# Kernel tuning notes

Measured on AMD Instinct MI355X. Metric: run time of the kernel, lower is better.

Reference implementation:

```python
import jax, jax.numpy as jnp
import numpy as np
import math

SEQ_LEN = 2048
D_MODEL = 1024
N_HEAD = 16
BATCH = 4


def setup_inputs() -> dict:
    key = jax.random.key(0)
    ks = jax.random.split(key, 12)
    D, T = D_MODEL, SEQ_LEN
    lin_bound = 1.0 / math.sqrt(D)  # torch nn.Linear default init
    xav_bound = math.sqrt(6.0 / (T + T))  # xavier_uniform for wbias
    u = lambda k, shape, b: jax.random.uniform(k, shape, jnp.float32, -b, b)
    return {
        "x": jax.random.normal(ks[0], (BATCH, T, D), jnp.float32),
        "dummy": 0,
        "Wq": u(ks[1], (D, D), lin_bound), "bq": u(ks[2], (D,), lin_bound),
        "Wk": u(ks[3], (D, D), lin_bound), "bk": u(ks[4], (D,), lin_bound),
        "Wv": u(ks[5], (D, D), lin_bound), "bv": u(ks[6], (D,), lin_bound),
        "Wo": u(ks[7], (D, D), lin_bound), "bo": u(ks[8], (D,), lin_bound),
        "wbias": u(ks[9], (T, T), xav_bound),
    }


def reference(x, dummy, Wq, bq, Wk, bk, Wv, bv, Wo, bo, wbias):
    B, T, D = x.shape
    H = N_HEAD
    dh = D // H

    def proj(W, b):
        # nn.Linear: x @ W.T + b, then view(B,T,H,dh) -> (B,H,T,dh)
        y = jnp.einsum('btd,ed->bte', x, W) + b
        return y.reshape(B, T, H, dh).transpose(0, 2, 1, 3)

    Q = proj(Wq, bq)
    K = proj(Wk, bk)
    V = proj(Wv, bv)

    ew = jnp.exp(wbias[:T, :T])          # [T,T] (unstabilized, as in torch src)
    eK = jnp.exp(K)                      # [B,H,T,dh]
    numer = jnp.einsum('ts,bhsd->bhtd', ew, eK * V)
    denom = jnp.einsum('ts,bhsd->bhtd', ew, eK)
    out = jax.nn.sigmoid(Q) * (numer / denom)   # [B,H,T,dh]
    out = out.transpose(0, 2, 1, 3).reshape(B, T, D)
    return jnp.einsum('btd,ed->bte', out, Wo) + bo
```

## Files before the change

### kernel.cpp

```cpp
#include <hip/hip_runtime.h>
#include <stdint.h>

typedef unsigned short u16;
typedef __attribute__((ext_vector_type(8))) short short8;
typedef __attribute__((ext_vector_type(4))) float f32x4;

#define SEQ 2048
#define DM 1024
#define NB 4
#define ROWS (NB*SEQ)

__device__ __forceinline__ u16 f2bf(float f) {
  union { float f; uint32_t u; } x; x.f = f;
  uint32_t u = x.u;
  uint32_t r = u + 0x7FFFu + ((u >> 16) & 1u);
  return (u16)(r >> 16);
}
__device__ __forceinline__ float bf2f(u16 h) {
  union { uint32_t u; float f; } x; x.u = ((uint32_t)h) << 16;
  return x.f;
}

__device__ __forceinline__ void g2l16(void* lds, const void* g) {
  __builtin_amdgcn_global_load_lds(
      (const __attribute__((address_space(1))) void*)g,
      (__attribute__((address_space(3))) void*)lds, 16, 0, 0);
}

__global__ void k_cvt_all(const float* __restrict__ x,
                          const float* __restrict__ Wq, const float* __restrict__ Wk,
                          const float* __restrict__ Wv, const float* __restrict__ Wo,
                          const float* __restrict__ wb, u16* __restrict__ dws) {
  int i = blockIdx.x * 256 + threadIdx.x;
  const float* src; long dst; bool ex = false;
  if (i < 2097152) { src = x + (long)i * 4; dst = (long)i * 4; }
  else if (i < 3145728) {
    int j = i - 2097152, which = j >> 18, o = j & 262143;
    const float* Wp = (which == 0) ? Wq : (which == 1) ? Wk : (which == 2) ? Wv : Wo;
    src = Wp + (long)o * 4; dst = 8388608 + (long)(j) * 4;
  } else { int j = i - 3145728; src = wb + (long)j * 4; dst = 12582912 + (long)j * 4; ex = true; }
  float4 v = *(const float4*)src;
  if (ex) { v.x = __expf(v.x); v.y = __expf(v.y); v.z = __expf(v.z); v.w = __expf(v.w); }
  ushort4 o4; o4.x = f2bf(v.x); o4.y = f2bf(v.y); o4.z = f2bf(v.z); o4.w = f2bf(v.w);
  *(ushort4*)(dws + dst) = o4;
}

#define SB __builtin_amdgcn_sched_barrier(0)

#define STAGE(t_, bf_) do { \
  _Pragma("unroll") for (int c = 0; c < 4; ++c) { \
    int idx = c * 512 + tid; \
    int r = idx >> 3; \
    int ce = ((idx & 7) ^ (r & 7)) * 8; \
    g2l16(&lds[(bf_)*BUFE + idx*8], Ag + (long)r*KD + (t_)*64 + ce); \
  } \
  _Pragma("unroll") for (int c = 0; c < BN/64; ++c) { \
    int idx = c * 512 + tid; \
    int r = idx >> 3; \
    int ce = ((idx & 7) ^ (r & 7)) * 8; \
    const u16* bp_ = (MODE == 3 && c >= 2) ? (Bg + 896L*KD) : Bg; \
    g2l16(&lds[(bf_)*BUFE + 16384 + idx*8], bp_ + (long)r*KD + (t_)*64 + ce); \
  } } while (0)

#define LDA8(d_, mh_) do { \
  _Pragma("unroll") for (int i = 0; i < FM/2; ++i) \
  _Pragma("unroll") for (int k = 0; k < 2; ++k) \
    d_[i][k] = *(const short8*)&lds[ab + ((mh_)*(RW/2) + i*16 + lr)*64 + 8*(((k<<2)|kg) ^ (lr&7))]; \
  } while (0)

#define LDB8(nh_) do { \
  _Pragma("unroll") for (int j = 0; j < 2; ++j) \
  _Pragma("unroll") for (int k = 0; k < 2; ++k) { \
    int rowB_ = (MODE == 3) ? ((nh_)*128 + wn*32 + j*16 + lr) \
                            : (wn*64 + ((nh_)*2+j)*16 + lr); \
    bn[nh_][j][k] = *(const short8*)&lds[bb + rowB_*64 + 8*(((k<<2)|kg) ^ (lr&7))]; \
  } } while (0)

#define MMC(d_, mh_, nh_) do { \
  __builtin_amdgcn_s_setprio(1); \
  _Pragma("unroll") for (int i = 0; i < FM/2; ++i) \
  _Pragma("unroll") for (int j = 0; j < 2; ++j) \
  _Pragma("unroll") for (int k = 0; k < 2; ++k) \
    acc[(mh_)*(FM/2)+i][(nh_)*2+j] = __builtin_amdgcn_mfma_f32_16x16x32_bf16( \
        d_[i][k], bn[nh_][j][k], acc[(mh_)*(FM/2)+i][(nh_)*2+j], 0, 0, 0); \
  __builtin_amdgcn_s_setprio(0); \
  } while (0)

template<int KD, int WM, int MODE>
__global__ __launch_bounds__(512)
void k_big(const u16* __restrict__ A, const u16* __restrict__ B,
           void* __restrict__ Cv,
           const float* __restrict__ b0, const float* __restrict__ b1,
           const float* __restrict__ b2, long sB, long sC)
{
  constexpr int WN = 8 / WM;
  constexpr int BN = WN * 64;
  constexpr int RW = 256 / WM;
  constexpr int FM = RW / 16;
  constexpr int NT = KD / 64;
  constexpr int BUFE = (256 + BN) * 64;
  __shared__ u16 lds[2 * BUFE];
  const int tid = threadIdx.x;
  const int l  = tid & 63, wid = tid >> 6;
  const int wm = wid / WN, wn = wid % WN;
  const int lr = l & 15,  kg = l >> 4;
  const int brow = blockIdx.y * 256;
  const int bcol = blockIdx.x * ((MODE == 3) ? 128 : BN);
  const u16* Ag = A + (long)brow * KD;
  const u16* Bg = B + (long)blockIdx.z * sB + (long)bcol * KD;

  f32x4 acc[FM][4];
#pragma unroll
  for (int m = 0; m < FM; ++m)
#pragma unroll
    for (int n = 0; n < 4; ++n) acc[m][n] = (f32x4){0.f, 0.f, 0.f, 0.f};

  short8 a0[FM/2][2], a1[FM/2][2], bn[2][2][2];

  STAGE(0, 0);
  STAGE(1, 1);

  for (int t = 0; t < NT; ++t) {
    const int bf = t & 1;
    if (t == NT - 1)              asm volatile("s_waitcnt vmcnt(0)" ::: "memory");
    else if constexpr (BN == 256) asm volatile("s_waitcnt vmcnt(8)" ::: "memory");
    else                          asm volatile("s_waitcnt vmcnt(6)" ::: "memory");
    __builtin_amdgcn_s_barrier();
    SB;
    const int ab = bf*BUFE + wm*RW*64;
    const int bb = bf*BUFE + 16384;
    LDA8(a0, 0); LDB8(0); SB;
    LDB8(1); SB;
    asm volatile("s_waitcnt lgkmcnt(4)" ::: "memory"); SB;
    MMC(a0, 0, 0);
    LDA8(a1, 1); SB;
    if constexpr (FM == 8) { asm volatile("s_waitcnt lgkmcnt(8)" ::: "memory"); }
    else                   { asm volatile("s_waitcnt lgkmcnt(4)" ::: "memory"); }
    SB;
    MMC(a0, 0, 1);
    asm volatile("s_waitcnt lgkmcnt(0)" ::: "memory"); SB;
    MMC(a1, 1, 1);
    MMC(a1, 1, 0);
    SB;
    __builtin_amdgcn_s_barrier();
    SB;
    if (t + 2 < NT) STAGE(t + 2, bf);
  }

  if constexpr (MODE == 3) {
    const u16* QsP = (const u16*)b0;
    u16* O = (u16*)Cv;
    const long rb = (long)blockIdx.z * 2048;
#pragma unroll
    for (int m = 0; m < FM; ++m)
#pragma unroll
      for (int j = 0; j < 2; ++j)
#pragma unroll
        for (int r = 0; r < 4; ++r) {
          int row = brow + wm*RW + m*16 + kg*4 + r;
          int e = bcol + wn*32 + j*16 + lr;
          float nu = acc[m][j][r];
          float de = acc[m][2+j][r];
          float q = bf2f(QsP[(rb + row) * 1024 + e]);
          O[(rb + row) * 1024 + e] = f2bf(q * nu * __builtin_amdgcn_rcpf(de));
        }
  } else {
#pragma unroll
    for (int m = 0; m < FM; ++m)
#pragma unroll
      for (int n = 0; n < 4; ++n)
#pragma unroll
        for (int r = 0; r < 4; ++r) {
          int row = brow + wm*RW + m*16 + kg*4 + r;
          int col = bcol + wn*64 + n*16 + lr;
          float v = acc[m][n][r];
          if (MODE == 1) {
            int seg = col >> 10, colr = col & 1023;
            const float* bp = (seg == 0) ? b0 : (seg == 1) ? b1 : b2;
            v += bp[colr];
            if (seg == 0) v = 1.f / (1.f + __expf(-v));
            ((u16*)Cv)[(long)seg * 8388608 + (long)row * 1024 + colr] = f2bf(v);
          } else {
            ((float*)Cv)[(long)row * 1024 + col] = v + b0[col];
          }
        }
  }
}

__global__ void k_trans(const u16* __restrict__ Kb, const u16* __restrict__ Vb,
                        u16* __restrict__ Z) {
  __shared__ u16 lk[64][65];
  __shared__ u16 lv[64][65];
  int s0 = blockIdx.x * 64, e0 = blockIdx.y * 64, b = blockIdx.z;
  int tx = threadIdx.x & 63, ty = threadIdx.x >> 6;
  const long baseIn = (long)b * SEQ * DM;
  for (int j = ty; j < 64; j += 4) {
    lk[j][tx] = Kb[baseIn + (long)(s0 + j) * DM + e0 + tx];
    lv[j][tx] = Vb[baseIn + (long)(s0 + j) * DM + e0 + tx];
  }
  __syncthreads();
  const long ob = (long)b * 2 * DM * SEQ;
  for (int j = ty; j < 64; j += 4) {
    int e = e0 + j;
    float kf = bf2f(lk[tx][j]);
    float vf = bf2f(lv[tx][j]);
    float ek = __expf(kf);
    Z[ob + (long)e * SEQ + s0 + tx]        = f2bf(ek * vf);
    Z[ob + (long)(DM + e) * SEQ + s0 + tx] = f2bf(ek);
  }
}

extern "C" void kernel_launch(void* const* d_in, const int* in_sizes, int n_in,
                              void* d_out, int out_size, void* d_ws, size_t ws_size,
                              hipStream_t stream)
{
  const float* x     = (const float*)d_in[0];
  const float* Wq    = (const float*)d_in[2];
  const float* bq    = (const float*)d_in[3];
  const float* Wk    = (const float*)d_in[4];
  const float* bk    = (const float*)d_in[5];
  const float* Wv    = (const float*)d_in[6];
  const float* bv    = (const float*)d_in[7];
  const float* Wo    = (const float*)d_in[8];
  const float* bo    = (const float*)d_in[9];
  const float* wbias = (const float*)d_in[10];

  char* ws = (char*)d_ws;
  u16*  xb  = (u16*)(ws);
  u16*  Wqb = (u16*)(ws + 16777216);
  u16*  Wob = (u16*)(ws + 16777216 + 3 * 2097152);
  u16*  EW  = (u16*)(ws + 25165824);
  u16*  Qs  = (u16*)(ws + 33554432);
  u16*  Kb  = (u16*)(ws + 50331648);
  u16*  Vb  = (u16*)(ws + 67108864);
  u16*  Z   = (u16*)(ws + 83886080);
  u16*  out1 = xb;

  k_cvt_all<<<16384, 256, 0, stream>>>(x, Wq, Wk, Wv, Wo, wbias, (u16*)ws);

  dim3 gqkv(3072 / 128, ROWS / 256, 1);
  k_big<1024, 4, 1><<<gqkv, 512, 0, stream>>>(xb, Wqb, Qs, bq, bk, bv, 0, 0);

  dim3 gt(SEQ / 64, DM / 64, NB);
  k_trans<<<gt, 256, 0, stream>>>(Kb, Vb, Z);

  dim3 g8(8, 8, NB);
  k_big<2048, 2, 3><<<g8, 512, 0, stream>>>(EW, Z, out1, (const float*)Qs,
                                            nullptr, nullptr,
                                            (long)2 * DM * SEQ, 0);

  dim3 gop(DM / 128, ROWS / 256, 1);
  k_big<1024, 4, 2><<<gop, 512, 0, stream>>>(out1, Wob, (float*)d_out, bo, nullptr,
                                             nullptr, 0, 0);
}
```

Baseline: 290.5 us.

## Fuse exp(K)*V transpose into QKV GEMM epilogue via interleaved K/V weight rows

The Wk and Wv rows are interleaved during weight conversion, so adjacent output columns of the QKV GEMM hold K and V for the same feature. The epilogue pairs them with a lane shuffle, computes exp(K) and exp(K)*V, and writes them transposed straight into the Z buffer. This removes the separate transpose kernel and the round trip of K and V through global memory. The main loop's wait schedule is also simplified to a full lgkmcnt(0) before each MFMA group, which may lose some overlap between LDS reads and matrix ops. The transposed 8-byte stores scattered across rows of Z may also coalesce poorly.

```diff
diff --git a/kernel.cpp b/kernel.cpp
--- a/kernel.cpp
+++ b/kernel.cpp
@@ -35,9 +35,12 @@
   const float* src; long dst; bool ex = false;
   if (i < 2097152) { src = x + (long)i * 4; dst = (long)i * 4; }
   else if (i < 3145728) {
-    int j = i - 2097152, which = j >> 18, o = j & 262143;
-    const float* Wp = (which == 0) ? Wq : (which == 1) ? Wk : (which == 2) ? Wv : Wo;
-    src = Wp + (long)o * 4; dst = 8388608 + (long)(j) * 4;
+    int j = i - 2097152, w = j >> 18, o = j & 262143;
+    const float* Wp = (w == 0) ? Wq : (w == 1) ? Wk : (w == 2) ? Wv : Wo;
+    src = Wp + (long)o * 4;
+    int e = o >> 8, c = o & 255;
+    int rowIdx = (w == 0) ? e : (w == 3) ? (3072 + e) : (1024 + 2 * e + (w - 1));
+    dst = 8388608 + (long)rowIdx * 1024 + c * 4;
   } else { int j = i - 3145728; src = wb + (long)j * 4; dst = 12582912 + (long)j * 4; ex = true; }
   float4 v = *(const float4*)src;
   if (ex) { v.x = __expf(v.x); v.y = __expf(v.y); v.z = __expf(v.z); v.w = __expf(v.w); }
@@ -76,7 +79,9 @@
     bn[nh_][j][k] = *(const short8*)&lds[bb + rowB_*64 + 8*(((k<<2)|kg) ^ (lr&7))]; \
   } } while (0)
 
-#define MMC(d_, mh_, nh_) do { \
+#define MM8(d_, mh_, nh_) do { \
+  asm volatile("s_waitcnt lgkmcnt(0)" ::: "memory"); \
+  SB; \
   __builtin_amdgcn_s_setprio(1); \
   _Pragma("unroll") for (int i = 0; i < FM/2; ++i) \
   _Pragma("unroll") for (int j = 0; j < 2; ++j) \
@@ -91,7 +96,8 @@
 void k_big(const u16* __restrict__ A, const u16* __restrict__ B,
            void* __restrict__ Cv,
            const float* __restrict__ b0, const float* __restrict__ b1,
-           const float* __restrict__ b2, long sB, long sC)
+           const float* __restrict__ b2, void* __restrict__ aux,
+           long sB, long sC)
 {
   constexpr int WN = 8 / WM;
   constexpr int BN = WN * 64;
@@ -129,18 +135,10 @@
     SB;
     const int ab = bf*BUFE + wm*RW*64;
     const int bb = bf*BUFE + 16384;
-    LDA8(a0, 0); LDB8(0); SB;
-    LDB8(1); SB;
-    asm volatile("s_waitcnt lgkmcnt(4)" ::: "memory"); SB;
-    MMC(a0, 0, 0);
-    LDA8(a1, 1); SB;
-    if constexpr (FM == 8) { asm volatile("s_waitcnt lgkmcnt(8)" ::: "memory"); }
-    else                   { asm volatile("s_waitcnt lgkmcnt(4)" ::: "memory"); }
-    SB;
-    MMC(a0, 0, 1);
-    asm volatile("s_waitcnt lgkmcnt(0)" ::: "memory"); SB;
-    MMC(a1, 1, 1);
-    MMC(a1, 1, 0);
+    LDA8(a0, 0); LDB8(0); MM8(a0, 0, 0);
+    LDB8(1);              MM8(a0, 0, 1);
+    LDA8(a1, 1);          MM8(a1, 1, 1);
+                          MM8(a1, 1, 0);
     SB;
     __builtin_amdgcn_s_barrier();
     SB;
@@ -164,6 +162,51 @@
           float q = bf2f(QsP[(rb + row) * 1024 + e]);
           O[(rb + row) * 1024 + e] = f2bf(q * nu * __builtin_amdgcn_rcpf(de));
         }
+  } else if constexpr (MODE == 1) {
+    if (bcol < 1024) {
+#pragma unroll
+      for (int m = 0; m < FM; ++m)
+#pragma unroll
+        for (int n = 0; n < 4; ++n)
+#pragma unroll
+          for (int r = 0; r < 4; ++r) {
+            int row = brow + wm*RW + m*16 + kg*4 + r;
+            int col = bcol + wn*64 + n*16 + lr;
+            float v = acc[m][n][r] + b0[col];
+            v = 1.f / (1.f + __expf(-v));
+            ((u16*)Cv)[(long)row * 1024 + col] = f2bf(v);
+          }
+    } else {
+      u16* Zp = (u16*)aux;
+      int colr = bcol + wn*64 - 1024;
+#pragma unroll
+      for (int m = 0; m < FM; ++m) {
+        int row0 = brow + wm*RW + m*16 + kg*4;
+        int b = row0 >> 11, s0 = row0 & 2047;
+        u16* Zb = Zp + (long)b * 2 * DM * SEQ;
+#pragma unroll
+        for (int n = 0; n < 4; ++n) {
+          int cl = colr + n*16 + lr;
+          int e = cl >> 1;
+          bool isK = (cl & 1) == 0;
+          float bias = isK ? b1[e] : b2[e];
+          ushort4 ekO, ekvO;
+#pragma unroll
+          for (int r = 0; r < 4; ++r) {
+            float vb = acc[m][n][r] + bias;
+            float partner = __shfl_xor(vb, 1);
+            float ek = __expf(vb);
+            float ekv = ek * partner;
+            ((u16*)&ekO)[r]  = f2bf(ek);
+            ((u16*)&ekvO)[r] = f2bf(ekv);
+          }
+          if (isK) {
+            *(ushort4*)&Zb[(long)(DM + e) * SEQ + s0] = ekO;
+            *(ushort4*)&Zb[(long)e * SEQ + s0]        = ekvO;
+          }
+        }
+      }
+    }
   } else {
 #pragma unroll
     for (int m = 0; m < FM; ++m)
@@ -173,40 +216,8 @@
         for (int r = 0; r < 4; ++r) {
           int row = brow + wm*RW + m*16 + kg*4 + r;
           int col = bcol + wn*64 + n*16 + lr;
-          float v = acc[m][n][r];
-          if (MODE == 1) {
-            int seg = col >> 10, colr = col & 1023;
-            const float* bp = (seg == 0) ? b0 : (seg == 1) ? b1 : b2;
-            v += bp[colr];
-            if (seg == 0) v = 1.f / (1.f + __expf(-v));
-            ((u16*)Cv)[(long)seg * 8388608 + (long)row * 1024 + colr] = f2bf(v);
-          } else {
-            ((float*)Cv)[(long)row * 1024 + col] = v + b0[col];
-          }
+          ((float*)Cv)[(long)row * 1024 + col] = acc[m][n][r] + b0[col];
         }
-  }
-}
-
-__global__ void k_trans(const u16* __restrict__ Kb, const u16* __restrict__ Vb,
-                        u16* __restrict__ Z) {
-  __shared__ u16 lk[64][65];
-  __shared__ u16 lv[64][65];
-  int s0 = blockIdx.x * 64, e0 = blockIdx.y * 64, b = blockIdx.z;
-  int tx = threadIdx.x & 63, ty = threadIdx.x >> 6;
-  const long baseIn = (long)b * SEQ * DM;
-  for (int j = ty; j < 64; j += 4) {
-    lk[j][tx] = Kb[baseIn + (long)(s0 + j) * DM + e0 + tx];
-    lv[j][tx] = Vb[baseIn + (long)(s0 + j) * DM + e0 + tx];
-  }
-  __syncthreads();
-  const long ob = (long)b * 2 * DM * SEQ;
-  for (int j = ty; j < 64; j += 4) {
-    int e = e0 + j;
-    float kf = bf2f(lk[tx][j]);
-    float vf = bf2f(lv[tx][j]);
-    float ek = __expf(kf);
-    Z[ob + (long)e * SEQ + s0 + tx]        = f2bf(ek * vf);
-    Z[ob + (long)(DM + e) * SEQ + s0 + tx] = f2bf(ek);
   }
 }
 
@@ -231,25 +242,20 @@
   u16*  Wob = (u16*)(ws + 16777216 + 3 * 2097152);
   u16*  EW  = (u16*)(ws + 25165824);
   u16*  Qs  = (u16*)(ws + 33554432);
-  u16*  Kb  = (u16*)(ws + 50331648);
-  u16*  Vb  = (u16*)(ws + 67108864);
   u16*  Z   = (u16*)(ws + 83886080);
   u16*  out1 = xb;
 
   k_cvt_all<<<16384, 256, 0, stream>>>(x, Wq, Wk, Wv, Wo, wbias, (u16*)ws);
 
   dim3 gqkv(3072 / 128, ROWS / 256, 1);
-  k_big<1024, 4, 1><<<gqkv, 512, 0, stream>>>(xb, Wqb, Qs, bq, bk, bv, 0, 0);
-
-  dim3 gt(SEQ / 64, DM / 64, NB);
-  k_trans<<<gt, 256, 0, stream>>>(Kb, Vb, Z);
+  k_big<1024, 4, 1><<<gqkv, 512, 0, stream>>>(xb, Wqb, Qs, bq, bk, bv, Z, 0, 0);
 
   dim3 g8(8, 8, NB);
   k_big<2048, 2, 3><<<g8, 512, 0, stream>>>(EW, Z, out1, (const float*)Qs,
-                                            nullptr, nullptr,
+                                            nullptr, nullptr, nullptr,
                                             (long)2 * DM * SEQ, 0);
 
   dim3 gop(DM / 128, ROWS / 256, 1);
   k_big<1024, 4, 2><<<gop, 512, 0, stream>>>(out1, Wob, (float*)d_out, bo, nullptr,
-                                             nullptr, 0, 0);
-}
+                                             nullptr, nullptr, 0, 0);
+}
```

Result: faster. 274.2 us (-5.6%).
